# Optimization experiments

Hardware: AMD Instinct MI355X
Metric: run time of the kernel (lower is better)

Reference implementation:

```python
import jax, jax.numpy as jnp
import numpy as np

B, S, H, EMB, VOCAB, LABEL, NUM_LAYERS = 32, 512, 256, 256, 32000, 16, 3


def _before(x):  # shift right along seq dim, zero-pad front
    z = jnp.zeros_like(x[:, :1])
    return jnp.concatenate([z, x[:, :-1]], axis=1)


def _after(x):  # shift left along seq dim, zero-pad end
    z = jnp.zeros_like(x[:, :1])
    return jnp.concatenate([x[:, 1:], z], axis=1)


def setup_inputs() -> dict:
    key = jax.random.key(0)
    ks = jax.random.split(key, 12)
    p = lambda k, shape: (0.02 * jax.random.normal(k, shape)).astype(jnp.float32)
    return {
        "span_nodes": jnp.zeros((1,), jnp.int32),
        "bert_vec": jnp.zeros((1,), jnp.float32),
        "node_text": jax.random.randint(ks[0], (B, S), 0, VOCAB),
        "word_mask": jnp.ones((B, S), jnp.float32),
        "sent_mask": jnp.ones((1,), jnp.int32),
        "node_feature": jnp.zeros((1,), jnp.float32),
        "adj": jnp.zeros((1,), jnp.int32),
        # embedding + emb_proj
        "E": p(ks[1], (VOCAB, EMB)),
        "Wp": p(ks[2], (EMB, H)), "bp": jnp.zeros((H,), jnp.float32),
        # SCell: W(3H->7H, no bias), U(emb->7H, no bias), V(H->7H, bias)
        "Ws": p(ks[3], (3 * H, 7 * H)), "Us": p(ks[4], (EMB, 7 * H)),
        "Vs": p(ks[5], (H, 7 * H)), "bVs": jnp.zeros((7 * H,), jnp.float32),
        # GCell: W(H->2H, no bias), w(H->H, no bias), U(H->2H, bias), u(H->H, bias)
        "WgW": p(ks[6], (H, 2 * H)), "Wgw": p(ks[7], (H, H)),
        "UgU": p(ks[8], (H, 2 * H)), "bgU": jnp.zeros((2 * H,), jnp.float32),
        "ugu": p(ks[9], (H, H)), "bgu": jnp.zeros((H,), jnp.float32),
        # output head
        "Wo": p(ks[10], (H, LABEL)), "bo": jnp.zeros((LABEL,), jnp.float32),
    }


def _slstm(node_text, word_mask, E, Wp, bp, Ws, Us, Vs, bVs,
           WgW, Wgw, UgU, bgU, ugu, bgu, Wo, bo):
    mask = word_mask[..., None]                      # [B,S,1]
    emb = E[node_text]                               # [B,S,EMB]
    proj = (emb @ Wp + bp) * mask                    # [B,S,H] (dropout=identity in eval)
    h = proj
    c = proj
    g = h.mean(1)                                    # [B,H]
    c_g = c.mean(1)                                  # [B,H]
    xU = emb @ Us                                    # [B,S,7H] hoisted (constant per layer)
    neg = ((1.0 - word_mask) * 1e16)[..., None]      # [B,S,1]
    for _ in range(NUM_LAYERS):
        h = h * mask
        c = c * mask
        # SCell
        hcat = jnp.concatenate([_before(h), h, _after(h)], axis=-1)   # [B,S,3H]
        gates = hcat @ Ws + xU + (g @ Vs + bVs)[:, None, :]           # [B,S,7H]
        gi, gl, gr, gf, gs, go, gu = jnp.split(gates, 7, axis=-1)
        gu = jnp.tanh(gu)
        # sigmoid then softmax over the stacked-gate dim (note: o stays raw, as in source)
        stk = jax.nn.softmax(jax.nn.sigmoid(jnp.stack([gi, gl, gr, gf, gs], axis=-2)), axis=-2)
        gi, gl, gr, gf, gs = (stk[..., k, :] for k in range(5))
        new_c = _before(c) * gl + c * gf + gr * _after(c) + gs * c_g[:, None, :] + gi * gu
        new_h = go * jnp.tanh(new_c)
        # GCell (uses pre-update h, c)
        h_avg = h.mean(1)                                             # [B,H]
        fo = jax.nn.sigmoid(g @ WgW + h_avg @ UgU + bgU)              # [B,2H]
        f_g, o_g = jnp.split(fo, 2, axis=-1)
        f_w = jax.nn.sigmoid((g @ Wgw)[:, None, :] + h @ ugu + bgu) - neg   # [B,S,H]
        f_w = jax.nn.softmax(f_w, axis=1)
        new_c_g = f_g * c_g + (c * f_w).sum(1)
        new_g = o_g * jnp.tanh(new_c_g)
        h, c, g, c_g = new_h, new_c, new_g, new_c_g
    return (g @ Wo + bo, g.mean(0) @ Wo + bo)


def reference(span_nodes, bert_vec, node_text, word_mask, sent_mask, node_feature, adj,
              E, Wp, bp, Ws, Us, Vs, bVs, WgW, Wgw, UgU, bgU, ugu, bgu, Wo, bo):
    return _slstm(node_text, word_mask, E, Wp, bp, Ws, Us, Vs, bVs,
                  WgW, Wgw, UgU, bgU, ugu, bgu, Wo, bo)
```

## Files before the change

kernel.cpp:

```cpp
#include <hip/hip_runtime.h>
#include <math.h>

#define B_      32
#define S_      512
#define H_      256
#define EMB_    256
#define M_      (B_*S_)
#define N7_     1792
#define NG_     2048
#define NS_     2560
#define KA_     1024
#define LABEL_  16

#define BM 256
#define BN 256
#define BK 64
#define NT (KA_/BK)
#define EBM 64

typedef __bf16 bf16x8 __attribute__((ext_vector_type(8)));
typedef float  f32x4  __attribute__((ext_vector_type(4)));
typedef unsigned short us8 __attribute__((ext_vector_type(8)));

__device__ __forceinline__ float sigf(float x){ return 1.f/(1.f+__expf(-x)); }

__device__ __forceinline__ unsigned short f2bf(float f){
    union { float f; unsigned int u; } v; v.f = f;
    unsigned int r = v.u + 0x7FFFu + ((v.u >> 16) & 1u);
    return (unsigned short)(r >> 16);
}
__device__ __forceinline__ float bf2f(unsigned short u){
    union { unsigned int i; float f; } v; v.i = ((unsigned int)u) << 16; return v.f;
}

#define WAUG_TH (NG_*KA_/8)
#define WPT_TH  (H_*EMB_/8)
#define EMB_TH  (M_*EMB_/8)
#define PREP_TH (WAUG_TH + WPT_TH + EMB_TH)

__global__ void prep_all(const float* __restrict__ Ws, const float* __restrict__ Us,
                         const float* __restrict__ ugu, const float* __restrict__ Wp,
                         const int* __restrict__ idx, const float* __restrict__ E,
                         unsigned short* __restrict__ WaugT, unsigned short* __restrict__ WpT,
                         unsigned short* __restrict__ embbf, unsigned short* __restrict__ zpage){
    long u = (long)blockIdx.x*256 + threadIdx.x;
    if(u < 512) zpage[u] = 0;
    if(u < WAUG_TH){
        int j  = (int)(u >> 7);
        int kc = ((int)u & 127) * 8;
        int tg = j >> 7, rem = j & 127, p = rem >> 4, t = tg*16 + (rem & 15);
        us8 o;
        if(p < 7){
            int col = p*256 + t;
            #pragma unroll
            for(int x=0;x<8;x++){
                int k = kc + x;
                float v = (k < 768) ? Ws[(long)k*N7_ + col] : Us[(long)(k-768)*N7_ + col];
                o[x] = f2bf(v);
            }
        } else {
            #pragma unroll
            for(int x=0;x<8;x++){
                int k = kc + x;
                float v = (k >= 256 && k < 512) ? ugu[(k-256)*H_ + t] : 0.f;
                o[x] = f2bf(v);
            }
        }
        *(us8*)&WaugT[(long)j*KA_ + kc] = o;
    } else if(u < WAUG_TH + WPT_TH){
        long v = u - WAUG_TH;
        int j = (int)(v >> 5), kc = ((int)v & 31)*8;
        us8 o;
        #pragma unroll
        for(int x=0;x<8;x++) o[x] = f2bf(Wp[(long)(kc+x)*H_ + j]);
        *(us8*)&WpT[(long)j*EMB_ + kc] = o;
    } else if(u < PREP_TH){
        long v = u - WAUG_TH - WPT_TH;
        int i = (int)(v >> 5), kc = ((int)v & 31)*8;
        const float* src = E + (size_t)idx[i]*EMB_ + kc;
        us8 o;
        #pragma unroll
        for(int x=0;x<8;x++) o[x] = f2bf(src[x]);
        *(us8*)&embbf[(size_t)i*EMB_ + kc] = o;
    }
}

__global__ __launch_bounds__(256, 2) void embed_mfma(
        const unsigned short* __restrict__ embbf, const unsigned short* __restrict__ WpT,
        const float* __restrict__ bp, const float* __restrict__ mask,
        unsigned short* __restrict__ h0b, float* __restrict__ c0){
    __shared__ unsigned short As[2][EBM*32];
    __shared__ unsigned short Bs[2][H_*32];
    int tid = threadIdx.x, w = tid>>6, l = tid&63, fr = l&15, fq = l>>4;
    int m0 = blockIdx.x * EBM;
    f32x4 acc[4][4];
    #pragma unroll
    for(int m=0;m<4;m++)
        #pragma unroll
        for(int n=0;n<4;n++) acc[m][n] = (f32x4){0.f,0.f,0.f,0.f};

    auto stage = [&](int buf, int kt){
        {
            int row = tid >> 2;
            int k0 = ((tid & 3) ^ ((row >> 1) & 3)) * 8;
            const unsigned short* src = embbf + (size_t)(m0+row)*EMB_ + kt + k0;
            __builtin_amdgcn_global_load_lds(
                (const __attribute__((address_space(1))) unsigned int*)src,
                (__attribute__((address_space(3))) unsigned int*)(&As[buf][w*512]),
                16, 0, 0);
        }
        #pragma unroll
        for(int q=0;q<4;q++){
            int v = q*256 + tid;
            int col = v >> 2;
            int k0 = ((v & 3) ^ ((col >> 1) & 3)) * 8;
            const unsigned short* src = WpT + (size_t)col*EMB_ + kt + k0;
            __builtin_amdgcn_global_load_lds(
                (const __attribute__((address_space(1))) unsigned int*)src,
                (__attribute__((address_space(3))) unsigned int*)(&Bs[buf][(q*256 + w*64)*8]),
                16, 0, 0);
        }
    };

    stage(0, 0);
    __syncthreads();
    int cur = 0;
    for(int step=0; step<EMB_/32; step++){
        if(step+1 < EMB_/32) stage(cur^1, (step+1)*32);
        bf16x8 bfv[4];
        #pragma unroll
        for(int n=0;n<4;n++){
            int colr = w*64 + n*16 + fr;
            int slot = fq ^ ((colr >> 1) & 3);
            bfv[n] = *(const bf16x8*)(&Bs[cur][colr*32 + slot*8]);
        }
        #pragma unroll
        for(int m=0;m<4;m++){
            int rowr = m*16 + fr;
            int slot = fq ^ ((rowr >> 1) & 3);
            bf16x8 af = *(const bf16x8*)(&As[cur][rowr*32 + slot*8]);
            #pragma unroll
            for(int n=0;n<4;n++)
                acc[m][n] = __builtin_amdgcn_mfma_f32_16x16x32_bf16(af, bfv[n], acc[m][n], 0,0,0);
        }
        __syncthreads();
        cur ^= 1;
    }
    #pragma unroll
    for(int m=0;m<4;m++){
        #pragma unroll
        for(int j=0;j<4;j++){
            int i = m0 + m*16 + fq*4 + j;
            float mk = mask[i];
            #pragma unroll
            for(int n=0;n<4;n++){
                int col = w*64 + n*16 + fr;
                float v = (acc[m][n][j] + bp[col]) * mk;
                h0b[(size_t)i*H_ + col] = f2bf(v);
                c0 [(size_t)i*H_ + col] = v;
            }
        }
    }
}

__global__ void reduce_mean_s(const unsigned short* __restrict__ h, float* __restrict__ outA,
                              float* __restrict__ outB){
    __shared__ float part[4][256];
    int b = blockIdx.x;
    int hh = threadIdx.x & 255, sg = threadIdx.x >> 8;
    float s = 0.f;
    long base = ((long)b*S_ + sg*128)*H_ + hh;
    for(int ss=0; ss<128; ss++) s += bf2f(h[base + (long)ss*H_]);
    part[sg][hh] = s;
    __syncthreads();
    if(threadIdx.x < 256){
        float t = (part[0][hh]+part[1][hh]+part[2][hh]+part[3][hh]) * (1.f/S_);
        outA[b*H_+hh] = t;
        if(outB) outB[b*H_+hh] = t;
    }
}

__global__ void small_gemm(const float* __restrict__ g, const float* __restrict__ havg,
                           const float* __restrict__ Vs, const float* __restrict__ bVs,
                           const float* __restrict__ Wgw, const float* __restrict__ bgu,
                           const float* __restrict__ WgW, const float* __restrict__ UgU,
                           const float* __restrict__ bgU, float* __restrict__ smalls){
    __shared__ float gs[256], hs[256];
    int b = blockIdx.y, t0 = threadIdx.x;
    gs[t0] = g[b*H_+t0];
    hs[t0] = havg[b*H_+t0];
    __syncthreads();
    int j = blockIdx.x*256 + t0;
    float acc;
    if(j < NG_){
        int tg = j >> 7, rem = j & 127, p = rem >> 4, t = tg*16 + (rem & 15);
        if(p < 7){
            int col = p*256 + t;
            acc = bVs[col];
            for(int k=0;k<H_;k++) acc += gs[k]*Vs[k*N7_+col];
        } else {
            acc = bgu[t];
            for(int k=0;k<H_;k++) acc += gs[k]*Wgw[k*H_+t];
        }
    } else {
        int jj = j - NG_;
        acc = bgU[jj];
        for(int k=0;k<H_;k++) acc += gs[k]*WgW[k*512+jj] + hs[k]*UgU[k*512+jj];
        acc = sigf(acc);
    }
    smalls[b*NS_+j] = acc;
}

__global__ __launch_bounds__(512, 2) void layer_mfma(
        const unsigned short* __restrict__ hbf, const unsigned short* __restrict__ embbf,
        const unsigned short* __restrict__ WaugT, const unsigned short* __restrict__ zpage,
        const float* __restrict__ c_old, const float* __restrict__ cg_old,
        const float* __restrict__ smalls, const float* __restrict__ mask,
        unsigned short* __restrict__ hbf_new, float* __restrict__ c_new,
        float* __restrict__ lpart, float* __restrict__ apart, float* __restrict__ hpart){
    __shared__ unsigned short As[2][BM*BK];
    __shared__ unsigned short Bs[2][BN*BK];
    __shared__ float red[8][16][3];
    int tid = threadIdx.x;
    int w = tid >> 6, l = tid & 63;
    int fr = l & 15, fq = l >> 4;
    int wr = w >> 1, wcl = w & 1;
    int m0 = blockIdx.x * BM;
    int n0 = blockIdx.y * BN;
    int b  = m0 >> 9;

    f32x4 acc[4][8];
    #pragma unroll
    for(int m=0;m<4;m++)
        #pragma unroll
        for(int n=0;n<8;n++) acc[m][n] = (f32x4){0.f,0.f,0.f,0.f};

    int rowc[2][2], k0a[2][2];
    #pragma unroll
    for(int p=0;p<2;p++)
        #pragma unroll
        for(int q=0;q<2;q++){
            int u = q*512 + tid;
            int row = p*128 + (u>>3);
            rowc[p][q] = row;
            k0a[p][q]  = ((u & 7) ^ (row & 7)) * 8;
        }
    const unsigned short* srcA[2][2];
    const unsigned short* srcB[2][2];
    #pragma unroll
    for(int hf=0;hf<2;hf++)
        #pragma unroll
        for(int q=0;q<2;q++){
            int u = q*512 + tid;
            int col = hf*128 + (u>>3);
            int k0 = ((u & 7) ^ (col & 7)) * 8;
            srcB[hf][q] = WaugT + (size_t)(n0 + col)*KA_ + k0;
        }
    auto setupA = [&](int r){
        #pragma unroll
        for(int p=0;p<2;p++)
            #pragma unroll
            for(int q=0;q<2;q++){
                int i = m0 + rowc[p][q];
                if(r < 3){
                    int si = (i & (S_-1)) + r - 1;
                    srcA[p][q] = ((unsigned)si < (unsigned)S_)
                               ? hbf + (size_t)(i + r - 1)*H_ + k0a[p][q]
                               : zpage + k0a[p][q];
                } else {
                    srcA[p][q] = embbf + (size_t)i*EMB_ + k0a[p][q];
                }
            }
    };
    auto advance = [&](){
        #pragma unroll
        for(int p=0;p<2;p++)
            #pragma unroll
            for(int q=0;q<2;q++){ srcA[p][q] += BK; srcB[p][q] += BK; }
    };
    auto stage_half = [&](int buf, int ph){
        if(ph < 2){
            #pragma unroll
            for(int q=0;q<2;q++)
                __builtin_amdgcn_global_load_lds(
                    (const __attribute__((address_space(1))) unsigned int*)srcA[ph][q],
                    (__attribute__((address_space(3))) unsigned int*)
                        (&As[buf][ph*8192 + (q*512 + w*64)*8]),
                    16, 0, 0);
        } else {
            int hf = ph - 2;
            #pragma unroll
            for(int q=0;q<2;q++)
                __builtin_amdgcn_global_load_lds(
                    (const __attribute__((address_space(1))) unsigned int*)srcB[hf][q],
                    (__attribute__((address_space(3))) unsigned int*)
                        (&Bs[buf][hf*8192 + (q*512 + w*64)*8]),
                    16, 0, 0);
        }
    };

    setupA(0);
    stage_half(0, 0); stage_half(0, 1); stage_half(0, 2); stage_half(0, 3);
    advance();

    bf16x8 afv[4];
    #pragma unroll 1
    for(int t=0; t<NT; ++t){
        int buf = t & 1;
        int st  = t + 1;
        if(st < NT){
            if((st & 3) == 0) setupA(st >> 2);
            stage_half(buf^1, 0);
            asm volatile("s_waitcnt vmcnt(2)" ::: "memory");
        } else {
            asm volatile("s_waitcnt vmcnt(0)" ::: "memory");
        }
        __builtin_amdgcn_s_barrier();
        #pragma unroll
        for(int p=0;p<4;p++){
            int ks = p >> 1, nh = p & 1;
            if(nh == 0){
                #pragma unroll
                for(int m=0;m<4;m++){
                    int row  = wr*64 + m*16 + fr;
                    int slot = (ks*4 + fq) ^ (row & 7);
                    afv[m] = *(const bf16x8*)(&As[buf][row*BK + slot*8]);
                }
            }
            bf16x8 bfv[4];
            #pragma unroll
            for(int nn=0;nn<4;nn++){
                int col  = wcl*128 + (nh*4+nn)*16 + fr;
                int slot = (ks*4 + fq) ^ (col & 7);
                bfv[nn] = *(const bf16x8*)(&Bs[buf][col*BK + slot*8]);
            }
            if(p < 3 && st < NT) stage_half(buf^1, p+1);
            __builtin_amdgcn_s_barrier();
            asm volatile("s_waitcnt lgkmcnt(0)" ::: "memory");
            __builtin_amdgcn_sched_barrier(0);
            __builtin_amdgcn_s_setprio(1);
            #pragma unroll
            for(int m=0;m<4;m++)
                #pragma unroll
                for(int nn=0;nn<4;nn++)
                    acc[m][nh*4+nn] = __builtin_amdgcn_mfma_f32_16x16x32_bf16(
                                          afv[m], bfv[nn], acc[m][nh*4+nn], 0,0,0);
            __builtin_amdgcn_s_setprio(0);
            __builtin_amdgcn_s_barrier();
        }
        if(st < NT) advance();
    }

    int t = (n0 >> 3) + wcl*16 + fr;
    float sm[8];
    #pragma unroll
    for(int n=0;n<8;n++) sm[n] = smalls[b*NS_ + n0 + wcl*128 + n*16 + fr];
    float cgv = cg_old[b*H_ + t];
    float lsum = 0.f, asum = 0.f, hsum = 0.f;
    #pragma unroll
    for(int m=0;m<4;m++){
        #pragma unroll
        for(int j=0;j<4;j++){
            int i = m0 + wr*64 + m*16 + fq*4 + j;
            int s = i & (S_-1);
            float gv[8];
            #pragma unroll
            for(int n=0;n<8;n++) gv[n] = acc[m][n][j] + sm[n];
            float ei=__expf(sigf(gv[0])), el=__expf(sigf(gv[1])), er=__expf(sigf(gv[2]));
            float ef=__expf(sigf(gv[3])), es=__expf(sigf(gv[4]));
            float inv = 1.f/(ei+el+er+ef+es);
            float c0v = c_old[(size_t)i*H_ + t];
            float cbv = (s>0)      ? c_old[(size_t)(i-1)*H_ + t] : 0.f;
            float cav = (s<S_-1)   ? c_old[(size_t)(i+1)*H_ + t] : 0.f;
            float tu = tanhf(gv[6]);
            float nc = (cbv*el + c0v*ef + er*cav + es*cgv + ei*tu)*inv;
            float nh2 = gv[5]*tanhf(nc);
            float mk = mask[i];
            float ncm = nc*mk, nhm = nh2*mk;
            c_new [(size_t)i*H_ + t] = ncm;
            hbf_new[(size_t)i*H_ + t] = f2bf(nhm);
            float e = __expf(sigf(gv[7]) - (1.f - mk)*1e16f);
            lsum += e;
            asum += e*c0v;
            hsum += nhm;
        }
    }
    #pragma unroll
    for(int off=16; off<64; off<<=1){
        lsum += __shfl_xor(lsum, off);
        asum += __shfl_xor(asum, off);
        hsum += __shfl_xor(hsum, off);
    }
    if(l < 16){ red[w][l][0]=lsum; red[w][l][1]=asum; red[w][l][2]=hsum; }
    __syncthreads();
    if(tid < 32){
        int wc2 = tid >> 4, fr2 = tid & 15;
        float L = 0.f, A = 0.f, Hh = 0.f;
        #pragma unroll
        for(int k=0;k<4;k++){
            L  += red[2*k + wc2][fr2][0];
            A  += red[2*k + wc2][fr2][1];
            Hh += red[2*k + wc2][fr2][2];
        }
        int tt = (n0 >> 3) + wc2*16 + fr2;
        int by = blockIdx.x;
        lpart[by*H_ + tt] = L;
        apart[by*H_ + tt] = A;
        hpart[by*H_ + tt] = Hh;
    }
}

__global__ void gcell2x(const float* __restrict__ lpart, const float* __restrict__ apart,
                        const float* __restrict__ hpart, const float* __restrict__ cg_old,
                        const float* __restrict__ smalls,
                        float* __restrict__ g_new, float* __restrict__ cg_new,
                        float* __restrict__ havg_out){
    int b = blockIdx.x, t = threadIdx.x;
    float L = 0.f, A = 0.f, Hs = 0.f;
    for(int ci=0; ci<2; ci++){
        int by = b*2 + ci;
        L  += lpart[by*H_ + t];
        A  += apart[by*H_ + t];
        Hs += hpart[by*H_ + t];
    }
    float fg = smalls[b*NS_ + NG_ + t];
    float og = smalls[b*NS_ + NG_ + 256 + t];
    float ncg = fg*cg_old[b*H_+t] + A/L;
    g_new[b*H_+t]    = og*tanhf(ncg);
    cg_new[b*H_+t]   = ncg;
    havg_out[b*H_+t] = Hs * (1.f/S_);
}

__global__ void outk(const float* __restrict__ g, const float* __restrict__ Wo,
                     const float* __restrict__ bo, float* __restrict__ out){
    __shared__ float o1[B_*LABEL_];
    int t = threadIdx.x;
    if(t < B_*LABEL_){
        int b = t/LABEL_, j = t%LABEL_;
        float acc = bo[j];
        for(int k=0;k<H_;k++) acc += g[b*H_+k]*Wo[k*LABEL_+j];
        o1[t] = acc;
        out[t] = acc;
    }
    __syncthreads();
    if(t < LABEL_){
        float s = 0.f;
        for(int b=0;b<B_;b++) s += o1[b*LABEL_+t];
        out[B_*LABEL_+t] = s*(1.f/B_);
    }
}

extern "C" void kernel_launch(void* const* d_in, const int* in_sizes, int n_in,
                              void* d_out, int out_size, void* d_ws, size_t ws_size,
                              hipStream_t stream){
    const int*   node_text = (const int*)  d_in[2];
    const float* word_mask = (const float*)d_in[3];
    const float* E   = (const float*)d_in[7];
    const float* Wp  = (const float*)d_in[8];
    const float* bp  = (const float*)d_in[9];
    const float* Ws  = (const float*)d_in[10];
    const float* Us  = (const float*)d_in[11];
    const float* Vs  = (const float*)d_in[12];
    const float* bVs = (const float*)d_in[13];
    const float* WgW = (const float*)d_in[14];
    const float* Wgw = (const float*)d_in[15];
    const float* UgU = (const float*)d_in[16];
    const float* bgU = (const float*)d_in[17];
    const float* ugu = (const float*)d_in[18];
    const float* bgu = (const float*)d_in[19];
    const float* Wo  = (const float*)d_in[20];
    const float* bo  = (const float*)d_in[21];

    float* w = (float*)d_ws;
    size_t off = 0;
    auto alloc = [&](size_t nfloats){ float* p = w + off; off += nfloats; return p; };
    unsigned short* WaugT = (unsigned short*)alloc((size_t)NG_*KA_/2);
    unsigned short* zpage = (unsigned short*)alloc(256);
    unsigned short* WpT   = (unsigned short*)alloc((size_t)H_*EMB_/2);
    unsigned short* embbf = (unsigned short*)alloc((size_t)M_*EMB_/2);
    unsigned short* hbf[2] = { (unsigned short*)alloc((size_t)M_*H_/2),
                               (unsigned short*)alloc((size_t)M_*H_/2) };
    float* cb[2]  = { alloc((size_t)M_*H_), alloc((size_t)M_*H_) };
    float* lpart  = alloc((size_t)(M_/BM)*H_);
    float* apart  = alloc((size_t)(M_/BM)*H_);
    float* hpart  = alloc((size_t)(M_/BM)*H_);
    float* gb[2]  = { alloc(B_*H_), alloc(B_*H_) };
    float* cgb[2] = { alloc(B_*H_), alloc(B_*H_) };
    float* havg   = alloc(B_*H_);
    float* smalls = alloc((size_t)B_*NS_);

    prep_all<<<(PREP_TH + 255)/256, 256, 0, stream>>>(Ws, Us, ugu, Wp, node_text, E,
                                                      WaugT, WpT, embbf, zpage);
    embed_mfma<<<M_/EBM, 256, 0, stream>>>(embbf, WpT, bp, word_mask, hbf[0], cb[0]);
    reduce_mean_s<<<B_, 1024, 0, stream>>>(hbf[0], gb[0], cgb[0]);

    int cur = 0;
    for(int layer=0; layer<3; layer++){
        int nxt = cur ^ 1;
        const float* havg_in = (layer == 0) ? gb[0] : havg;
        small_gemm<<<dim3(NS_/256, B_), 256, 0, stream>>>(gb[cur], havg_in, Vs, bVs,
                                                          Wgw, bgu, WgW, UgU, bgU, smalls);
        layer_mfma<<<dim3(M_/BM, NG_/BN), 512, 0, stream>>>(hbf[cur], embbf, WaugT, zpage,
                                                            cb[cur], cgb[cur], smalls, word_mask,
                                                            hbf[nxt], cb[nxt],
                                                            lpart, apart, hpart);
        gcell2x<<<B_, 256, 0, stream>>>(lpart, apart, hpart, cgb[cur], smalls,
                                        gb[nxt], cgb[nxt], havg);
        cur = nxt;
    }
    outk<<<1, 512, 0, stream>>>(gb[cur], Wo, bo, (float*)d_out);
}
```

Measured before the change: 383.5 us.

## Batch small GEMM over 8 rows, widen weight prep, restage layer pipeline

The small GEMM now processes 8 batch rows per block, so each weight load is reused 8 times and far fewer blocks re-read the Vs/UgU matrices. The weight-prep kernel has each thread handle 32 k-values for one output column, which makes consecutive threads read consecutive columns and gives coalesced reads of Ws/Us. The main MFMA loop moves the wait and barrier to the top of each K-step and spreads the four stage_half loads evenly across the four sub-phases, adding a sched_barrier after the MFMAs. The new wait is vmcnt(0) instead of vmcnt(2), which can reduce load/compute overlap.

```diff
diff --git a/kernel.cpp b/kernel.cpp
--- a/kernel.cpp
+++ b/kernel.cpp
@@ -33,7 +33,7 @@
     union { unsigned int i; float f; } v; v.i = ((unsigned int)u) << 16; return v.f;
 }
 
-#define WAUG_TH (NG_*KA_/8)
+#define WAUG_TH (NG_*(KA_/32))
 #define WPT_TH  (H_*EMB_/8)
 #define EMB_TH  (M_*EMB_/8)
 #define PREP_TH (WAUG_TH + WPT_TH + EMB_TH)
@@ -46,27 +46,32 @@
     long u = (long)blockIdx.x*256 + threadIdx.x;
     if(u < 512) zpage[u] = 0;
     if(u < WAUG_TH){
-        int j  = (int)(u >> 7);
-        int kc = ((int)u & 127) * 8;
+        int j  = (int)u & (NG_-1);
+        int kb = ((int)u >> 11) * 32;
         int tg = j >> 7, rem = j & 127, p = rem >> 4, t = tg*16 + (rem & 15);
-        us8 o;
+        us8 o[4];
         if(p < 7){
             int col = p*256 + t;
             #pragma unroll
-            for(int x=0;x<8;x++){
-                int k = kc + x;
-                float v = (k < 768) ? Ws[(long)k*N7_ + col] : Us[(long)(k-768)*N7_ + col];
-                o[x] = f2bf(v);
-            }
+            for(int c=0;c<4;c++)
+                #pragma unroll
+                for(int x=0;x<8;x++){
+                    int k = kb + c*8 + x;
+                    float v = (k < 768) ? Ws[(long)k*N7_ + col] : Us[(long)(k-768)*N7_ + col];
+                    o[c][x] = f2bf(v);
+                }
         } else {
             #pragma unroll
-            for(int x=0;x<8;x++){
-                int k = kc + x;
-                float v = (k >= 256 && k < 512) ? ugu[(k-256)*H_ + t] : 0.f;
-                o[x] = f2bf(v);
-            }
-        }
-        *(us8*)&WaugT[(long)j*KA_ + kc] = o;
+            for(int c=0;c<4;c++)
+                #pragma unroll
+                for(int x=0;x<8;x++){
+                    int k = kb + c*8 + x;
+                    float v = (k >= 256 && k < 512) ? ugu[(k-256)*H_ + t] : 0.f;
+                    o[c][x] = f2bf(v);
+                }
+        }
+        #pragma unroll
+        for(int c=0;c<4;c++) *(us8*)&WaugT[(long)j*KA_ + kb + c*8] = o[c];
     } else if(u < WAUG_TH + WPT_TH){
         long v = u - WAUG_TH;
         int j = (int)(v >> 5), kc = ((int)v & 31)*8;
@@ -180,35 +185,56 @@
     }
 }
 
-__global__ void small_gemm(const float* __restrict__ g, const float* __restrict__ havg,
-                           const float* __restrict__ Vs, const float* __restrict__ bVs,
-                           const float* __restrict__ Wgw, const float* __restrict__ bgu,
-                           const float* __restrict__ WgW, const float* __restrict__ UgU,
-                           const float* __restrict__ bgU, float* __restrict__ smalls){
-    __shared__ float gs[256], hs[256];
-    int b = blockIdx.y, t0 = threadIdx.x;
-    gs[t0] = g[b*H_+t0];
-    hs[t0] = havg[b*H_+t0];
+__global__ void small_gemm2(const float* __restrict__ g, const float* __restrict__ havg,
+                            const float* __restrict__ Vs, const float* __restrict__ bVs,
+                            const float* __restrict__ Wgw, const float* __restrict__ bgu,
+                            const float* __restrict__ WgW, const float* __restrict__ UgU,
+                            const float* __restrict__ bgU, float* __restrict__ smalls){
+    __shared__ float gs[8][256], hs[8][256];
+    int t0 = threadIdx.x;
+    int b0 = blockIdx.y * 8;
+    #pragma unroll
+    for(int q=0;q<8;q++){
+        gs[q][t0] = g[(b0+q)*H_ + t0];
+        hs[q][t0] = havg[(b0+q)*H_ + t0];
+    }
     __syncthreads();
     int j = blockIdx.x*256 + t0;
-    float acc;
+    float acc[8];
     if(j < NG_){
         int tg = j >> 7, rem = j & 127, p = rem >> 4, t = tg*16 + (rem & 15);
         if(p < 7){
             int col = p*256 + t;
-            acc = bVs[col];
-            for(int k=0;k<H_;k++) acc += gs[k]*Vs[k*N7_+col];
+            #pragma unroll
+            for(int q=0;q<8;q++) acc[q] = bVs[col];
+            for(int k=0;k<H_;k++){
+                float wv = Vs[k*N7_+col];
+                #pragma unroll
+                for(int q=0;q<8;q++) acc[q] += gs[q][k]*wv;
+            }
         } else {
-            acc = bgu[t];
-            for(int k=0;k<H_;k++) acc += gs[k]*Wgw[k*H_+t];
-        }
+            #pragma unroll
+            for(int q=0;q<8;q++) acc[q] = bgu[t];
+            for(int k=0;k<H_;k++){
+                float wv = Wgw[k*H_+t];
+                #pragma unroll
+                for(int q=0;q<8;q++) acc[q] += gs[q][k]*wv;
+            }
+        }
+        #pragma unroll
+        for(int q=0;q<8;q++) smalls[(b0+q)*NS_ + j] = acc[q];
     } else {
         int jj = j - NG_;
-        acc = bgU[jj];
-        for(int k=0;k<H_;k++) acc += gs[k]*WgW[k*512+jj] + hs[k]*UgU[k*512+jj];
-        acc = sigf(acc);
-    }
-    smalls[b*NS_+j] = acc;
+        #pragma unroll
+        for(int q=0;q<8;q++) acc[q] = bgU[jj];
+        for(int k=0;k<H_;k++){
+            float w1 = WgW[k*512+jj], w2 = UgU[k*512+jj];
+            #pragma unroll
+            for(int q=0;q<8;q++) acc[q] += gs[q][k]*w1 + hs[q][k]*w2;
+        }
+        #pragma unroll
+        for(int q=0;q<8;q++) smalls[(b0+q)*NS_ + j] = sigf(acc[q]);
+    }
 }
 
 __global__ __launch_bounds__(512, 2) void layer_mfma(
@@ -308,17 +334,13 @@
     for(int t=0; t<NT; ++t){
         int buf = t & 1;
         int st  = t + 1;
-        if(st < NT){
-            if((st & 3) == 0) setupA(st >> 2);
-            stage_half(buf^1, 0);
-            asm volatile("s_waitcnt vmcnt(2)" ::: "memory");
-        } else {
-            asm volatile("s_waitcnt vmcnt(0)" ::: "memory");
-        }
-        __builtin_amdgcn_s_barrier();
         #pragma unroll
         for(int p=0;p<4;p++){
             int ks = p >> 1, nh = p & 1;
+            if(p == 0){
+                asm volatile("s_waitcnt vmcnt(0)" ::: "memory");
+                __builtin_amdgcn_s_barrier();
+            }
             if(nh == 0){
                 #pragma unroll
                 for(int m=0;m<4;m++){
@@ -334,7 +356,10 @@
                 int slot = (ks*4 + fq) ^ (col & 7);
                 bfv[nn] = *(const bf16x8*)(&Bs[buf][col*BK + slot*8]);
             }
-            if(p < 3 && st < NT) stage_half(buf^1, p+1);
+            if(st < NT){
+                if(p == 0 && (st & 3) == 0) setupA(st >> 2);
+                stage_half(buf^1, p);
+            }
             __builtin_amdgcn_s_barrier();
             asm volatile("s_waitcnt lgkmcnt(0)" ::: "memory");
             __builtin_amdgcn_sched_barrier(0);
@@ -346,6 +371,7 @@
                     acc[m][nh*4+nn] = __builtin_amdgcn_mfma_f32_16x16x32_bf16(
                                           afv[m], bfv[nn], acc[m][nh*4+nn], 0,0,0);
             __builtin_amdgcn_s_setprio(0);
+            __builtin_amdgcn_sched_barrier(0);
             __builtin_amdgcn_s_barrier();
         }
         if(st < NT) advance();
@@ -498,7 +524,7 @@
     for(int layer=0; layer<3; layer++){
         int nxt = cur ^ 1;
         const float* havg_in = (layer == 0) ? gb[0] : havg;
-        small_gemm<<<dim3(NS_/256, B_), 256, 0, stream>>>(gb[cur], havg_in, Vs, bVs,
+        small_gemm2<<<dim3(NS_/256, 4), 256, 0, stream>>>(gb[cur], havg_in, Vs, bVs,
                                                           Wgw, bgu, WgW, UgU, bgU, smalls);
         layer_mfma<<<dim3(M_/BM, NG_/BN), 512, 0, stream>>>(hbf[cur], embbf, WaugT, zpage,
                                                             cb[cur], cgb[cur], smalls, word_mask,
```

After: 434.2 us. 1.13x slower.
